# Kernel tuning notes

Measured on AMD Instinct MI355X. Metric: run time of the kernel, lower is better.

Reference implementation:

```python
import jax, jax.numpy as jnp
import numpy as np

N = 32768       # nodes
IN = 256        # in_channels
D = 128         # out_channels (per-head dim)
H = 4           # num_heads
M = 4           # num_reps (seeds per partition)
KP = 128        # number of partitions
S = N // KP     # partition size (equal-size partitions)
SCALE = float(np.sqrt(D))


def _linear_init(key, fan_in, fan_out):
    # torch nn.Linear default: U(-1/sqrt(fan_in), 1/sqrt(fan_in)) for W and b
    kw, kb = jax.random.split(key)
    bound = 1.0 / np.sqrt(fan_in)
    w = jax.random.uniform(kw, (fan_in, fan_out), jnp.float32, -bound, bound)
    b = jax.random.uniform(kb, (fan_out,), jnp.float32, -bound, bound)
    return w, b


def setup_inputs() -> dict:
    key = jax.random.key(0)
    k0, k1, k2, k3, k4 = jax.random.split(key, 5)
    x = jax.random.normal(k0, (N, IN), jnp.float32)
    # equal-size disjoint partitions: [KP, S] index array covering 0..N-1
    partition_indices = jnp.arange(N, dtype=jnp.int32).reshape(KP, S)
    Wq_w, Wq_b = _linear_init(k1, IN, H * D)
    Wk_w, Wk_b = _linear_init(k2, IN, H * D)
    Wv_w, Wv_b = _linear_init(k3, IN, H * D)
    pool_seeds = jax.random.normal(k4, (M, H, D), jnp.float32) * 0.02
    alpha_logit = jnp.float32(0.0)
    beta = jnp.float32(1.0)
    return {
        "x": x, "partition_indices": partition_indices,
        "Wq_w": Wq_w, "Wq_b": Wq_b, "Wk_w": Wk_w, "Wk_b": Wk_b,
        "Wv_w": Wv_w, "Wv_b": Wv_b, "pool_seeds": pool_seeds,
        "alpha_logit": alpha_logit, "beta": beta,
    }


def reference(x, partition_indices, Wq_w, Wq_b, Wk_w, Wk_b, Wv_w, Wv_b,
              pool_seeds, alpha_logit, beta):
    n = x.shape[0]
    Q = (x @ Wq_w + Wq_b).reshape(n, H, D)
    K = (x @ Wk_w + Wk_b).reshape(n, H, D)
    V = (x @ Wv_w + Wv_b).reshape(n, H, D)

    # gather per partition -> [KP, S, H, D]
    Qp = Q[partition_indices]
    Kp = K[partition_indices]
    Vp = V[partition_indices]

    # Fine: exact softmax attention within each partition
    attn_local = jnp.einsum('kphd,kqhd->khpq', Qp, Kp) / SCALE
    attn_local = jax.nn.softmax(attn_local, axis=-1)
    outp = jnp.einsum('khpq,kqhd->kphd', attn_local, Vp)  # [KP,S,H,D]
    # partitions are disjoint -> scatter-set back to node order
    out_local = jnp.zeros((n, H, D), x.dtype).at[partition_indices.reshape(-1)].set(
        outp.reshape(n, H, D))
    x_local = out_local.mean(axis=1)  # [N, D]

    # Coarse: learned seeds pool each partition
    pool_attn = jnp.einsum('mhd,kqhd->kmhq', pool_seeds, Kp) / SCALE
    pool_attn = jax.nn.softmax(pool_attn, axis=-1)
    reps_k = jnp.einsum('kmhq,kqhd->kmhd', pool_attn, Kp).reshape(KP * M, H, D)
    reps_v = jnp.einsum('kmhq,kqhd->kmhd', pool_attn, Vp).reshape(KP * M, H, D)

    # Global cross-attention: every node attends to all partition reps
    cross_attn = jnp.einsum('nhd,rhd->nhr', Q, reps_k) / SCALE
    cross_attn = jax.nn.softmax(cross_attn, axis=-1)
    out_global = jnp.einsum('nhr,rhd->nhd', cross_attn, reps_v)
    x_global = out_global.mean(axis=1)  # [N, D]

    x_self = V.mean(axis=1)
    alpha = jax.nn.sigmoid(alpha_logit)
    return alpha * x_local + (1.0 - alpha) * x_global + beta * x_self
```

## Files before the change

### kernel.cpp

```cpp
#include <hip/hip_runtime.h>
#include <hip/hip_bf16.h>


#define INV_SCALE 0.08838834764831845f

typedef __attribute__((ext_vector_type(8))) short bf16x8;
typedef __attribute__((ext_vector_type(4))) float floatx4;
typedef unsigned short ushort_t;
typedef unsigned int uint32;

#define OFF_Q    0ull
#define OFF_K    33554432ull
#define OFF_V    67108864ull
#define OFF_LOC  100663296ull
#define OFF_RPK  109051904ull
#define OFF_XC   110100480ull
#define OFF_WC   126877696ull
#define OFF_SCAL 127671296ull
#define OFF_FLAG 127671304ull
#define OFF_RVT  127672320ull
#define OFF_GLB  128196608ull

#define WC_WQ 0
#define WC_WK 131072
#define WC_WV 262144
#define WC_BQ 393216
#define WC_BK 393728
#define WC_BV 394240
#define WC_SEED 394752
#define WC_TOT 396800

static __device__ __forceinline__ float bflo(uint32 u) {
  return __uint_as_float(u << 16);
}
static __device__ __forceinline__ float bfhi(uint32 u) {
  return __uint_as_float(u & 0xffff0000u);
}
static __device__ __forceinline__ float bf2f(ushort_t u) {
  return __uint_as_float(((uint32)u) << 16);
}
static __device__ __forceinline__ ushort_t f2bf(float f) {
  uint32 x = __float_as_uint(f);
  uint32 r = x + 0x7fffu + ((x >> 16) & 1u);
  return (ushort_t)(r >> 16);
}
static __device__ __forceinline__ uint32 pack2bf(float a, float b) {
  return (uint32)f2bf(a) | ((uint32)f2bf(b) << 16);
}

__global__ __launch_bounds__(64) void k_detect(const uint32* __restrict__ xw,
                                               const ushort_t* __restrict__ betaRaw,
                                               uint32* __restrict__ flags) {
  const int lane = threadIdx.x;
  const uint32 w = xw[lane * 137 + 3];
  const int e = (w >> 7) & 0xff;
  const unsigned long long b = __ballot(e >= 100 && e <= 140);
  if (lane == 0) {
    flags[0] = (__popcll(b) >= 48) ? 1u : 0u;
    flags[1] = (betaRaw[0] != 0) ? 1u : 0u;
  }
}

static __device__ __forceinline__ void conv8(const void* src, long j, int isB,
                                             ushort_t* dst) {
  if (isB) {
    *reinterpret_cast<uint4*>(dst) =
        *reinterpret_cast<const uint4*>(reinterpret_cast<const ushort_t*>(src) + j);
  } else {
    const float* f = reinterpret_cast<const float*>(src) + j;
    const float4 a = *reinterpret_cast<const float4*>(f);
    const float4 b = *reinterpret_cast<const float4*>(f + 4);
    uint4 o;
    o.x = pack2bf(a.x, a.y); o.y = pack2bf(a.z, a.w);
    o.z = pack2bf(b.x, b.y); o.w = pack2bf(b.z, b.w);
    *reinterpret_cast<uint4*>(dst) = o;
  }
}

__global__ __launch_bounds__(256) void k_convert(
    const void* __restrict__ x,
    const void* __restrict__ Wq, const void* __restrict__ bq,
    const void* __restrict__ Wk, const void* __restrict__ bk,
    const void* __restrict__ Wv, const void* __restrict__ bv,
    const void* __restrict__ seeds, const void* __restrict__ alpha,
    const void* __restrict__ beta,
    ushort_t* __restrict__ xc, ushort_t* __restrict__ wc,
    float* __restrict__ scal, const uint32* __restrict__ flags)
{
  const int isB = (int)flags[0];
  const long i8 = ((long)blockIdx.x * 256 + threadIdx.x) * 8;
  if (blockIdx.y == 0) {
    conv8(x, i8, isB, xc + i8);
  } else {
    if (i8 < WC_BQ) {
      const int sel = (int)(i8 >> 17);
      const long local = i8 & 131071;
      const int kk = (int)(local >> 9);
      const int nn = (int)(local & 511);
      const void* src = sel == 0 ? Wq : (sel == 1 ? Wk : Wv);
      ushort_t* dstW = wc + sel * 131072;
#pragma unroll
      for (int j = 0; j < 8; ++j) {
        ushort_t v;
        if (isB) v = reinterpret_cast<const ushort_t*>(src)[local + j];
        else     v = f2bf(reinterpret_cast<const float*>(src)[local + j]);
        dstW[(size_t)(nn + j) * 256 + kk] = v;
      }
    } else if (i8 < WC_TOT) {
      const void* src; long j;
      if (i8 < WC_BK)        { src = bq;    j = i8 - WC_BQ; }
      else if (i8 < WC_BV)   { src = bk;    j = i8 - WC_BK; }
      else if (i8 < WC_SEED) { src = bv;    j = i8 - WC_BV; }
      else                   { src = seeds; j = i8 - WC_SEED; }
      conv8(src, j, isB, wc + i8);
    }
    if (blockIdx.x == 0 && threadIdx.x == 0) {
      const int isBS = (int)flags[1];
      scal[0] = isBS ? bf2f(reinterpret_cast<const ushort_t*>(alpha)[0])
                     : reinterpret_cast<const float*>(alpha)[0];
      scal[1] = isBS ? bf2f(reinterpret_cast<const ushort_t*>(beta)[0])
                     : reinterpret_cast<const float*>(beta)[0];
    }
  }
}

__global__ __launch_bounds__(256) void k_qkv(
    const ushort_t* __restrict__ xc, const ushort_t* __restrict__ wc,
    ushort_t* __restrict__ Qb, ushort_t* __restrict__ Kb, ushort_t* __restrict__ Vb)
{
  const int m0 = blockIdx.x * 64;
  const int tid = threadIdx.x, lane = tid & 63, wv = tid >> 6;
  const int l16 = lane & 15, quad = lane >> 4;

  __shared__ __align__(16) ushort_t Xs[64 * 256];
  __shared__ __align__(16) ushort_t Ws[64 * 256];

#pragma unroll
  for (int i = 0; i < 8; ++i) {
    const int id = tid + 256 * i;
    const int row = id >> 5, c = id & 31;
    uint4 v = *reinterpret_cast<const uint4*>(xc + (size_t)(m0 + row) * 256 + c * 8);
    *reinterpret_cast<uint4*>(&Xs[row * 256 + ((c ^ (row & 7)) << 3)]) = v;
  }

  for (int sel = 0; sel < 3; ++sel) {
    const ushort_t* WT   = wc + sel * 131072;
    const ushort_t* bias = wc + WC_BQ + sel * 512;
    ushort_t* out        = sel == 0 ? Qb : (sel == 1 ? Kb : Vb);
    for (int nc = 0; nc < 8; ++nc) {
      const int n0 = nc * 64;
      __syncthreads();
#pragma unroll
      for (int i = 0; i < 8; ++i) {
        const int id = tid + 256 * i;
        const int row = id >> 5, c = id & 31;
        uint4 v = *reinterpret_cast<const uint4*>(WT + (size_t)(n0 + row) * 256 + c * 8);
        *reinterpret_cast<uint4*>(&Ws[row * 256 + ((c ^ (row & 7)) << 3)]) = v;
      }
      __syncthreads();

      floatx4 acc[4] = {};
      const int arow = wv * 16 + l16;
#pragma unroll
      for (int ks = 0; ks < 8; ++ks) {
        const int ac = ks * 4 + quad;
        bf16x8 a = *reinterpret_cast<const bf16x8*>(&Xs[arow * 256 + ((ac ^ (arow & 7)) << 3)]);
#pragma unroll
        for (int nt = 0; nt < 4; ++nt) {
          const int brow = nt * 16 + l16;
          bf16x8 b = *reinterpret_cast<const bf16x8*>(&Ws[brow * 256 + ((ac ^ (brow & 7)) << 3)]);
          acc[nt] = __builtin_amdgcn_mfma_f32_16x16x32_bf16(a, b, acc[nt], 0, 0, 0);
        }
      }

#pragma unroll
      for (int nt = 0; nt < 4; ++nt) {
        const int col = n0 + nt * 16 + l16;
        const float bf = bf2f(bias[col]);
#pragma unroll
        for (int r = 0; r < 4; ++r) {
          const int row = m0 + wv * 16 + quad * 4 + r;
          out[(size_t)row * 512 + col] = f2bf(acc[nt][r] + bf);
        }
      }
    }
  }
}

__global__ __launch_bounds__(256) void k_pool(
    const ushort_t* __restrict__ Kb, const ushort_t* __restrict__ Vb,
    const int* __restrict__ pidx_all, const ushort_t* __restrict__ wc,
    ushort_t* __restrict__ rpk, ushort_t* __restrict__ rvT)
{
  const int k = blockIdx.x, h = blockIdx.y;
  const int tid = threadIdx.x, lane = tid & 63, wv = tid >> 6;
  const int* pidx = pidx_all + k * 256;

  __shared__ __align__(16) ushort_t SB[128 * 256];
  const uint32* SBU = reinterpret_cast<const uint32*>(SB);

#pragma unroll
  for (int i = 0; i < 16; ++i) {
    const int e8 = tid + 256 * i;
    const int q = e8 >> 4, dc = (e8 & 15) * 8;
    uint4 kv = *reinterpret_cast<const uint4*>(Kb + (size_t)pidx[q] * 512 + h * 128 + dc);
    const ushort_t* ku = reinterpret_cast<const ushort_t*>(&kv);
    const int qp = q >> 1, qb = q & 1;
#pragma unroll
    for (int j = 0; j < 8; ++j) {
      const int d = dc + j;
      SB[d * 256 + (((qp ^ (d & 31)) << 1) | qb)] = ku[j];
    }
  }
  __syncthreads();

  float q00, q01, q10, q11;
  {
    const uint32* ssrc = reinterpret_cast<const uint32*>(wc + WC_SEED + (size_t)(wv * 4 + h) * 128);
    float s00 = 0.f, s01 = 0.f, s10 = 0.f, s11 = 0.f;
#pragma unroll 8
    for (int dc = 0; dc < 64; ++dc) {
      const uint32 qv = ssrc[dc];
      const float a0 = bflo(qv), a1 = bfhi(qv);
      const int d0 = dc * 2, d1 = d0 + 1;
      const int c0 = lane ^ (d0 & 31);
      const int c1 = lane ^ (d1 & 31);
      const uint32 u00 = SBU[d0 * 128 + c0];
      const uint32 u01 = SBU[d0 * 128 + c0 + 64];
      const uint32 u10 = SBU[d1 * 128 + c1];
      const uint32 u11 = SBU[d1 * 128 + c1 + 64];
      s00 += a0 * bflo(u00) + a1 * bflo(u10);
      s01 += a0 * bfhi(u00) + a1 * bfhi(u10);
      s10 += a0 * bflo(u01) + a1 * bflo(u11);
      s11 += a0 * bfhi(u01) + a1 * bfhi(u11);
    }
    s00 *= INV_SCALE; s01 *= INV_SCALE; s10 *= INV_SCALE; s11 *= INV_SCALE;
    float mx = fmaxf(fmaxf(s00, s01), fmaxf(s10, s11));
#pragma unroll
    for (int off = 32; off >= 1; off >>= 1) mx = fmaxf(mx, __shfl_xor(mx, off));
    const float e00 = __expf(s00 - mx), e01 = __expf(s01 - mx);
    const float e10 = __expf(s10 - mx), e11 = __expf(s11 - mx);
    float sm = e00 + e01 + e10 + e11;
#pragma unroll
    for (int off = 32; off >= 1; off >>= 1) sm += __shfl_xor(sm, off);
    const float inv = 1.0f / sm;
    q00 = e00 * inv; q01 = e01 * inv; q10 = e10 * inv; q11 = e11 * inv;
  }

  {
    float rk0 = 0.f, rk1 = 0.f;
    const int d0 = 2 * lane, d1 = 2 * lane + 1;
#pragma unroll 4
    for (int qp = 0; qp < 64; ++qp) {
      const float pa = __shfl(q00, qp), pb = __shfl(q01, qp);
      const float pc = __shfl(q10, qp), pd = __shfl(q11, qp);
      const int c0 = qp ^ (d0 & 31);
      const int c1 = qp ^ (d1 & 31);
      const uint32 u0  = SBU[d0 * 128 + c0];
      const uint32 u0b = SBU[d0 * 128 + c0 + 64];
      const uint32 u1  = SBU[d1 * 128 + c1];
      const uint32 u1b = SBU[d1 * 128 + c1 + 64];
      rk0 += pa * bflo(u0) + pb * bfhi(u0) + pc * bflo(u0b) + pd * bfhi(u0b);
      rk1 += pa * bflo(u1) + pb * bfhi(u1) + pc * bflo(u1b) + pd * bfhi(u1b);
    }
    reinterpret_cast<uint32*>(rpk + ((size_t)((k * 4 + wv) * 4 + h)) * 128)[lane] = pack2bf(rk0, rk1);
  }
  __syncthreads();

#pragma unroll
  for (int i = 0; i < 16; ++i) {
    const int e8 = tid + 256 * i;
    const int q = e8 >> 4, dc = (e8 & 15) * 8;
    uint4 vv = *reinterpret_cast<const uint4*>(Vb + (size_t)pidx[q] * 512 + h * 128 + dc);
    *reinterpret_cast<uint4*>(&SB[q * 128 + dc]) = vv;
  }
  __syncthreads();

  {
    float rv0 = 0.f, rv1 = 0.f;
#pragma unroll 4
    for (int qp = 0; qp < 64; ++qp) {
      const float pa = __shfl(q00, qp), pb = __shfl(q01, qp);
      const float pc = __shfl(q10, qp), pd = __shfl(q11, qp);
      const uint32 v00 = SBU[(2 * qp) * 64 + lane];
      const uint32 v01 = SBU[(2 * qp + 1) * 64 + lane];
      const uint32 v10 = SBU[(128 + 2 * qp) * 64 + lane];
      const uint32 v11 = SBU[(129 + 2 * qp) * 64 + lane];
      rv0 += pa * bflo(v00) + pb * bflo(v01) + pc * bflo(v10) + pd * bflo(v11);
      rv1 += pa * bfhi(v00) + pb * bfhi(v01) + pc * bfhi(v10) + pd * bfhi(v11);
    }
    const int rrep = k * 4 + wv;
    rvT[(size_t)(h * 128 + 2 * lane) * 512 + rrep]     = f2bf(rv0);
    rvT[(size_t)(h * 128 + 2 * lane + 1) * 512 + rrep] = f2bf(rv1);
  }
}

__global__ __launch_bounds__(256) void k_fine(
    const ushort_t* __restrict__ Qb, const ushort_t* __restrict__ Kb,
    const ushort_t* __restrict__ Vb, const int* __restrict__ pidx_all,
    ushort_t* __restrict__ locS)
{
  const int k = blockIdx.x, qg = blockIdx.y;
  const int tid = threadIdx.x, lane = tid & 63, wv = tid >> 6;
  const int l16 = lane & 15, quad = lane >> 4;
  const int* pidx = pidx_all + k * 256;

  __shared__ __align__(16) ushort_t Qs[64 * 136];
  __shared__ __align__(16) ushort_t SB2[64 * 136];
  __shared__ __align__(16) ushort_t Ps[4][16 * 72];

  float accS[8][4];
#pragma unroll
  for (int nt = 0; nt < 8; ++nt)
#pragma unroll
    for (int r = 0; r < 4; ++r) accS[nt][r] = 0.f;

  for (int h = 0; h < 4; ++h) {
    __syncthreads();
#pragma unroll
    for (int i = 0; i < 4; ++i) {
      const int e = tid + 256 * i;
      const int r = e >> 4, c8 = (e & 15) * 8;
      uint4 v = *reinterpret_cast<const uint4*>(Qb + (size_t)pidx[qg * 64 + r] * 512 + h * 128 + c8);
      *reinterpret_cast<uint4*>(&Qs[r * 136 + c8]) = v;
    }

    floatx4 O[8] = {};
    float m_i[4], l_i[4];
#pragma unroll
    for (int r = 0; r < 4; ++r) { m_i[r] = -3e38f; l_i[r] = 0.f; }

    for (int c = 0; c < 4; ++c) {
      __syncthreads();
#pragma unroll
      for (int i = 0; i < 4; ++i) {
        const int e = tid + 256 * i;
        const int r = e >> 4, c8 = (e & 15) * 8;
        uint4 v = *reinterpret_cast<const uint4*>(Kb + (size_t)pidx[c * 64 + r] * 512 + h * 128 + c8);
        *reinterpret_cast<uint4*>(&SB2[r * 136 + c8]) = v;
      }
      __syncthreads();

      floatx4 S[4] = {};
#pragma unroll
      for (int ks = 0; ks < 4; ++ks) {
        bf16x8 a = *reinterpret_cast<const bf16x8*>(&Qs[(wv * 16 + l16) * 136 + ks * 32 + quad * 8]);
#pragma unroll
        for (int nt = 0; nt < 4; ++nt) {
          bf16x8 b = *reinterpret_cast<const bf16x8*>(&SB2[(nt * 16 + l16) * 136 + ks * 32 + quad * 8]);
          S[nt] = __builtin_amdgcn_mfma_f32_16x16x32_bf16(a, b, S[nt], 0, 0, 0);
        }
      }
#pragma unroll
      for (int nt = 0; nt < 4; ++nt)
#pragma unroll
        for (int r = 0; r < 4; ++r) S[nt][r] *= INV_SCALE;

#pragma unroll
      for (int r = 0; r < 4; ++r) {
        float cm = fmaxf(fmaxf(S[0][r], S[1][r]), fmaxf(S[2][r], S[3][r]));
#pragma unroll
        for (int off = 1; off <= 8; off <<= 1) cm = fmaxf(cm, __shfl_xor(cm, off));
        const float mn = fmaxf(m_i[r], cm);
        const float sc = __expf(m_i[r] - mn);
        m_i[r] = mn;
        l_i[r] *= sc;
#pragma unroll
        for (int nt = 0; nt < 8; ++nt) O[nt][r] *= sc;
        float ps = 0.f;
#pragma unroll
        for (int nt = 0; nt < 4; ++nt) {
          const float p = __expf(S[nt][r] - mn);
          ps += p;
          Ps[wv][(quad * 4 + r) * 72 + nt * 16 + l16] = f2bf(p);
        }
#pragma unroll
        for (int off = 1; off <= 8; off <<= 1) ps += __shfl_xor(ps, off);
        l_i[r] += ps;
      }
      __syncthreads();

#pragma unroll
      for (int i = 0; i < 4; ++i) {
        const int e = tid + 256 * i;
        const int key = e & 63, dc8 = (e >> 6) * 8;
        uint4 vv = *reinterpret_cast<const uint4*>(Vb + (size_t)pidx[c * 64 + key] * 512 + h * 128 + dc8);
        const ushort_t* u = reinterpret_cast<const ushort_t*>(&vv);
#pragma unroll
        for (int j = 0; j < 8; ++j) {
          const int d = dc8 + j;
          SB2[d * 64 + (((key >> 3) ^ j) << 3) + (key & 7)] = u[j];
        }
      }
      __syncthreads();

#pragma unroll
      for (int ks = 0; ks < 2; ++ks) {
        bf16x8 a = *reinterpret_cast<const bf16x8*>(&Ps[wv][l16 * 72 + ks * 32 + quad * 8]);
#pragma unroll
        for (int nt = 0; nt < 8; ++nt) {
          const int d = nt * 16 + l16;
          const int q8 = ks * 4 + quad;
          bf16x8 b = *reinterpret_cast<const bf16x8*>(&SB2[d * 64 + ((q8 ^ (d & 7)) << 3)]);
          O[nt] = __builtin_amdgcn_mfma_f32_16x16x32_bf16(a, b, O[nt], 0, 0, 0);
        }
      }
    }

#pragma unroll
    for (int r = 0; r < 4; ++r) {
      const float inv = 1.0f / l_i[r];
#pragma unroll
      for (int nt = 0; nt < 8; ++nt) accS[nt][r] += O[nt][r] * inv;
    }
  }

#pragma unroll
  for (int r = 0; r < 4; ++r) {
    const int n = pidx[qg * 64 + wv * 16 + quad * 4 + r];
#pragma unroll
    for (int nt = 0; nt < 8; ++nt)
      locS[(size_t)n * 128 + nt * 16 + l16] = f2bf(accS[nt][r] * 0.25f);
  }
}

__global__ __launch_bounds__(256) void k_cross(
    const ushort_t* __restrict__ Qb, const ushort_t* __restrict__ rpk,
    const ushort_t* __restrict__ rvT, ushort_t* __restrict__ glb)
{
  const int h = blockIdx.y;
  const int n0 = blockIdx.x * 64;
  const int tid = threadIdx.x, lane = tid & 63, wv = tid >> 6;
  const int l16 = lane & 15, quad = lane >> 4;

  __shared__ __align__(16) ushort_t Qs[64 * 136];
  __shared__ __align__(16) ushort_t Bs[128 * 72];
  __shared__ __align__(16) ushort_t Ps[4][16 * 72];

#pragma unroll
  for (int i = 0; i < 4; ++i) {
    const int e = tid + 256 * i;
    const int r = e >> 4, c8 = (e & 15) * 8;
    uint4 v = *reinterpret_cast<const uint4*>(Qb + (size_t)(n0 + r) * 512 + h * 128 + c8);
    *reinterpret_cast<uint4*>(&Qs[r * 136 + c8]) = v;
  }

  floatx4 O[8] = {};
  float m_i[4], l_i[4];
#pragma unroll
  for (int r = 0; r < 4; ++r) { m_i[r] = -3e38f; l_i[r] = 0.f; }

  for (int c = 0; c < 8; ++c) {
    __syncthreads();
#pragma unroll
    for (int i = 0; i < 4; ++i) {
      const int e = tid + 256 * i;
      const int r = e >> 4, c8 = (e & 15) * 8;
      uint4 v = *reinterpret_cast<const uint4*>(rpk + ((size_t)((c * 64 + r) * 4 + h)) * 128 + c8);
      *reinterpret_cast<uint4*>(&Bs[r * 136 + c8]) = v;
    }
    __syncthreads();

    floatx4 S[4] = {};
#pragma unroll
    for (int ks = 0; ks < 4; ++ks) {
      bf16x8 a = *reinterpret_cast<const bf16x8*>(&Qs[(wv * 16 + l16) * 136 + ks * 32 + quad * 8]);
#pragma unroll
      for (int nt = 0; nt < 4; ++nt) {
        bf16x8 b = *reinterpret_cast<const bf16x8*>(&Bs[(nt * 16 + l16) * 136 + ks * 32 + quad * 8]);
        S[nt] = __builtin_amdgcn_mfma_f32_16x16x32_bf16(a, b, S[nt], 0, 0, 0);
      }
    }
#pragma unroll
    for (int nt = 0; nt < 4; ++nt)
#pragma unroll
      for (int r = 0; r < 4; ++r) S[nt][r] *= INV_SCALE;

#pragma unroll
    for (int r = 0; r < 4; ++r) {
      float cm = fmaxf(fmaxf(S[0][r], S[1][r]), fmaxf(S[2][r], S[3][r]));
#pragma unroll
      for (int off = 1; off <= 8; off <<= 1) cm = fmaxf(cm, __shfl_xor(cm, off));
      const float mn = fmaxf(m_i[r], cm);
      const float sc = __expf(m_i[r] - mn);
      m_i[r] = mn;
      l_i[r] *= sc;
#pragma unroll
      for (int nt = 0; nt < 8; ++nt) O[nt][r] *= sc;
      float ps = 0.f;
#pragma unroll
      for (int nt = 0; nt < 4; ++nt) {
        const float p = __expf(S[nt][r] - mn);
        ps += p;
        Ps[wv][(quad * 4 + r) * 72 + nt * 16 + l16] = f2bf(p);
      }
#pragma unroll
      for (int off = 1; off <= 8; off <<= 1) ps += __shfl_xor(ps, off);
      l_i[r] += ps;
    }
    __syncthreads();

#pragma unroll
    for (int i = 0; i < 4; ++i) {
      const int e = tid + 256 * i;
      const int d = e >> 3, c8 = (e & 7) * 8;
      uint4 v = *reinterpret_cast<const uint4*>(rvT + ((size_t)(h * 128 + d)) * 512 + c * 64 + c8);
      *reinterpret_cast<uint4*>(&Bs[d * 72 + c8]) = v;
    }
    __syncthreads();

#pragma unroll
    for (int ks = 0; ks < 2; ++ks) {
      bf16x8 a = *reinterpret_cast<const bf16x8*>(&Ps[wv][l16 * 72 + ks * 32 + quad * 8]);
#pragma unroll
      for (int nt = 0; nt < 8; ++nt) {
        bf16x8 b = *reinterpret_cast<const bf16x8*>(&Bs[(nt * 16 + l16) * 72 + ks * 32 + quad * 8]);
        O[nt] = __builtin_amdgcn_mfma_f32_16x16x32_bf16(a, b, O[nt], 0, 0, 0);
      }
    }
  }

#pragma unroll
  for (int r = 0; r < 4; ++r) {
    const float inv = 1.0f / l_i[r];
    const int n = n0 + wv * 16 + quad * 4 + r;
#pragma unroll
    for (int nt = 0; nt < 8; ++nt)
      glb[(size_t)n * 512 + h * 128 + nt * 16 + l16] = f2bf(O[nt][r] * inv);
  }
}

__global__ __launch_bounds__(256) void k_combine(
    const ushort_t* __restrict__ locS, const ushort_t* __restrict__ glb,
    const ushort_t* __restrict__ Vb, const float* __restrict__ scal,
    float* __restrict__ out)
{
  const int t = blockIdx.x * 256 + threadIdx.x;
  const int n = t >> 6, dp = t & 63;
  const float alpha = 1.0f / (1.0f + __expf(-scal[0]));
  const float beta = scal[1];
  const uint32 lv = reinterpret_cast<const uint32*>(locS)[(size_t)n * 64 + dp];
  float g0 = 0.f, g1 = 0.f, v0 = 0.f, v1 = 0.f;
#pragma unroll
  for (int hh = 0; hh < 4; ++hh) {
    const uint32 gv = *reinterpret_cast<const uint32*>(glb + (size_t)n * 512 + hh * 128 + 2 * dp);
    const uint32 vv = *reinterpret_cast<const uint32*>(Vb + (size_t)n * 512 + hh * 128 + 2 * dp);
    g0 += bflo(gv); g1 += bfhi(gv);
    v0 += bflo(vv); v1 += bfhi(vv);
  }
  const float r0 = alpha * bflo(lv) + (1.0f - alpha) * g0 * 0.25f + beta * v0 * 0.25f;
  const float r1 = alpha * bfhi(lv) + (1.0f - alpha) * g1 * 0.25f + beta * v1 * 0.25f;
  reinterpret_cast<float2*>(out)[(size_t)n * 64 + dp] = make_float2(r0, r1);
}

extern "C" void kernel_launch(void* const* d_in, const int* in_sizes, int n_in,
                              void* d_out, int out_size, void* d_ws, size_t ws_size,
                              hipStream_t stream) {
  const void* x     = d_in[0];
  const int*  pidx  = (const int*)d_in[1];
  const void* Wq    = d_in[2];
  const void* bq    = d_in[3];
  const void* Wk    = d_in[4];
  const void* bk    = d_in[5];
  const void* Wv    = d_in[6];
  const void* bv    = d_in[7];
  const void* seeds = d_in[8];
  const void* al    = d_in[9];
  const void* be    = d_in[10];

  char* ws = (char*)d_ws;
  ushort_t* Qb   = (ushort_t*)(ws + OFF_Q);
  ushort_t* Kb   = (ushort_t*)(ws + OFF_K);
  ushort_t* Vb   = (ushort_t*)(ws + OFF_V);
  ushort_t* locS = (ushort_t*)(ws + OFF_LOC);
  ushort_t* rpk  = (ushort_t*)(ws + OFF_RPK);
  ushort_t* xc   = (ushort_t*)(ws + OFF_XC);
  ushort_t* wc   = (ushort_t*)(ws + OFF_WC);
  float*    scal = (float*)   (ws + OFF_SCAL);
  uint32*   flags= (uint32*)  (ws + OFF_FLAG);
  ushort_t* rvT  = (ushort_t*)(ws + OFF_RVT);
  ushort_t* glb  = (ushort_t*)(ws + OFF_GLB);

  k_detect<<<1, 64, 0, stream>>>((const uint32*)x, (const ushort_t*)be, flags);
  k_convert<<<dim3(4096, 2), 256, 0, stream>>>(x, Wq, bq, Wk, bk, Wv, bv, seeds, al, be,
                                               xc, wc, scal, flags);
  k_qkv<<<512, 256, 0, stream>>>(xc, wc, Qb, Kb, Vb);
  k_pool<<<dim3(128, 4), 256, 0, stream>>>(Kb, Vb, pidx, wc, rpk, rvT);
  k_fine<<<dim3(128, 4), 256, 0, stream>>>(Qb, Kb, Vb, pidx, locS);
  k_cross<<<dim3(512, 4), 256, 0, stream>>>(Qb, rpk, rvT, glb);
  k_combine<<<8192, 256, 0, stream>>>(locS, glb, Vb, scal, (float*)d_out);
}
```

Measured before the change: 381.8 us.

## Load cross-attention operands directly from global memory, drop LDS staging and barriers

```diff
diff --git a/kernel.cpp b/kernel.cpp
--- a/kernel.cpp
+++ b/kernel.cpp
@@ -424,7 +424,7 @@
   }
 }
 
-__global__ __launch_bounds__(256) void k_cross(
+__global__ __launch_bounds__(256, 4) void k_cross(
     const ushort_t* __restrict__ Qb, const ushort_t* __restrict__ rpk,
     const ushort_t* __restrict__ rvT, ushort_t* __restrict__ glb)
 {
@@ -433,17 +433,19 @@
   const int tid = threadIdx.x, lane = tid & 63, wv = tid >> 6;
   const int l16 = lane & 15, quad = lane >> 4;
 
-  __shared__ __align__(16) ushort_t Qs[64 * 136];
-  __shared__ __align__(16) ushort_t Bs[128 * 72];
   __shared__ __align__(16) ushort_t Ps[4][16 * 72];
 
-#pragma unroll
-  for (int i = 0; i < 4; ++i) {
-    const int e = tid + 256 * i;
-    const int r = e >> 4, c8 = (e & 15) * 8;
-    uint4 v = *reinterpret_cast<const uint4*>(Qb + (size_t)(n0 + r) * 512 + h * 128 + c8);
-    *reinterpret_cast<uint4*>(&Qs[r * 136 + c8]) = v;
-  }
+  bf16x8 qf[4];
+  {
+    const ushort_t* qrow =
+        Qb + (size_t)(n0 + wv * 16 + l16) * 512 + h * 128 + quad * 8;
+#pragma unroll
+    for (int ks = 0; ks < 4; ++ks)
+      qf[ks] = *reinterpret_cast<const bf16x8*>(qrow + ks * 32);
+  }
+
+  const ushort_t* rpkB = rpk + (size_t)l16 * 512 + h * 128 + quad * 8;
+  const ushort_t* rvtB = rvT + ((size_t)(h * 128 + l16)) * 512 + quad * 8;
 
   floatx4 O[8] = {};
   float m_i[4], l_i[4];
@@ -451,24 +453,14 @@
   for (int r = 0; r < 4; ++r) { m_i[r] = -3e38f; l_i[r] = 0.f; }
 
   for (int c = 0; c < 8; ++c) {
-    __syncthreads();
-#pragma unroll
-    for (int i = 0; i < 4; ++i) {
-      const int e = tid + 256 * i;
-      const int r = e >> 4, c8 = (e & 15) * 8;
-      uint4 v = *reinterpret_cast<const uint4*>(rpk + ((size_t)((c * 64 + r) * 4 + h)) * 128 + c8);
-      *reinterpret_cast<uint4*>(&Bs[r * 136 + c8]) = v;
-    }
-    __syncthreads();
-
     floatx4 S[4] = {};
 #pragma unroll
     for (int ks = 0; ks < 4; ++ks) {
-      bf16x8 a = *reinterpret_cast<const bf16x8*>(&Qs[(wv * 16 + l16) * 136 + ks * 32 + quad * 8]);
 #pragma unroll
       for (int nt = 0; nt < 4; ++nt) {
-        bf16x8 b = *reinterpret_cast<const bf16x8*>(&Bs[(nt * 16 + l16) * 136 + ks * 32 + quad * 8]);
-        S[nt] = __builtin_amdgcn_mfma_f32_16x16x32_bf16(a, b, S[nt], 0, 0, 0);
+        bf16x8 b = *reinterpret_cast<const bf16x8*>(
+            rpkB + ((size_t)(c * 64 + nt * 16)) * 512 + ks * 32);
+        S[nt] = __builtin_amdgcn_mfma_f32_16x16x32_bf16(qf[ks], b, S[nt], 0, 0, 0);
       }
     }
 #pragma unroll
@@ -498,23 +490,14 @@
       for (int off = 1; off <= 8; off <<= 1) ps += __shfl_xor(ps, off);
       l_i[r] += ps;
     }
-    __syncthreads();
-
-#pragma unroll
-    for (int i = 0; i < 4; ++i) {
-      const int e = tid + 256 * i;
-      const int d = e >> 3, c8 = (e & 7) * 8;
-      uint4 v = *reinterpret_cast<const uint4*>(rvT + ((size_t)(h * 128 + d)) * 512 + c * 64 + c8);
-      *reinterpret_cast<uint4*>(&Bs[d * 72 + c8]) = v;
-    }
-    __syncthreads();
 
 #pragma unroll
     for (int ks = 0; ks < 2; ++ks) {
       bf16x8 a = *reinterpret_cast<const bf16x8*>(&Ps[wv][l16 * 72 + ks * 32 + quad * 8]);
 #pragma unroll
       for (int nt = 0; nt < 8; ++nt) {
-        bf16x8 b = *reinterpret_cast<const bf16x8*>(&Bs[(nt * 16 + l16) * 72 + ks * 32 + quad * 8]);
+        bf16x8 b = *reinterpret_cast<const bf16x8*>(
+            rvtB + ((size_t)(nt * 16)) * 512 + c * 64 + ks * 32);
         O[nt] = __builtin_amdgcn_mfma_f32_16x16x32_bf16(a, b, O[nt], 0, 0, 0);
       }
     }
```

Result: slower. 525.9 us (+37.8%).
